# Optimization experiments

Hardware: AMD Instinct MI355X
Metric: run time of the kernel (lower is better)

Reference implementation:

```python
import jax, jax.numpy as jnp
import numpy as np

VOCAB = 50257
EMB = 256
HID = 256
FORGET_BIAS = 1.0


def setup_inputs() -> dict:
    key = jax.random.key(0)
    ks = jax.random.split(key, 8)
    B, T = 16, 256
    s = 0.05
    return {
        "tokens": jax.random.randint(ks[0], (B, T), 0, VOCAB, dtype=jnp.int32),
        # embedding matrix init mimics tf.random_uniform(-1, 1)
        "emb": jax.random.uniform(ks[1], (VOCAB, EMB), jnp.float32, -1.0, 1.0),
        "W1": jax.random.normal(ks[2], (EMB + HID, 4 * HID), jnp.float32) * s,
        "b1": jnp.zeros((4 * HID,), jnp.float32),
        "W2": jax.random.normal(ks[3], (HID + HID, 4 * HID), jnp.float32) * s,
        "b2": jnp.zeros((4 * HID,), jnp.float32),
        "Wout": jax.random.normal(ks[4], (HID, VOCAB), jnp.float32) * s,
        "bout": jnp.zeros((VOCAB,), jnp.float32),
    }


def _lstm_cell(c, h, x, W, b):
    # BasicLSTMCell: gates = [x, h] @ W + b, split i, j, f, o
    g = jnp.concatenate([x, h], axis=-1) @ W + b
    i, j, f, o = jnp.split(g, 4, axis=-1)
    c_new = c * jax.nn.sigmoid(f + FORGET_BIAS) + jax.nn.sigmoid(i) * jnp.tanh(j)
    h_new = jnp.tanh(c_new) * jax.nn.sigmoid(o)
    return c_new, h_new


def reference(tokens, emb, W1, b1, W2, b2, Wout, bout):
    B, T = tokens.shape
    x = emb[tokens]                 # [B, T, EMB] embedding lookup
    x_tm = jnp.swapaxes(x, 0, 1)    # [T, B, EMB] time-major for scan

    def step(carry, xt):
        c1, h1, c2, h2 = carry
        c1, h1 = _lstm_cell(c1, h1, xt, W1, b1)
        c2, h2 = _lstm_cell(c2, h2, h1, W2, b2)
        return (c1, h1, c2, h2), h2

    z = jnp.zeros((B, HID), x.dtype)
    _, hs = jax.lax.scan(step, (z, z, z, z), x_tm)  # hs: [T, B, HID]
    hs = jnp.swapaxes(hs, 0, 1).reshape(-1, HID)    # [B*T, HID] (batch-major flatten as in tf.reshape)
    logits = hs @ Wout + bout                        # [B*T, VOCAB]
    return logits
```

## Files before the change

### kernel.cpp

```cpp
#include <hip/hip_runtime.h>
#include <hip/hip_bf16.h>
#include <stdint.h>

#define BB 16
#define TT 256
#define HH 256
#define EE 256
#define GG 1024
#define VV 50257
#define NN 4096
#define NWK 352
#define NTILE 12608

typedef unsigned short u16;
typedef __attribute__((ext_vector_type(8))) short short8;
typedef __attribute__((ext_vector_type(4))) float f32x4;

__device__ __forceinline__ float sigm(float x){
    float e = __builtin_amdgcn_exp2f(fminf(-x*1.44269504f, 60.0f));
    return 1.0f/(1.0f+e);
}
__device__ __forceinline__ float tanha(float x){
    float e = __builtin_amdgcn_exp2f(fminf(x*2.885390082f, 60.0f));
    return (e-1.0f)/(e+1.0f);
}
__device__ __forceinline__ u16 f2bf(float f){
    uint32_t u = __float_as_uint(f);
    u = (u + 0x7FFFu + ((u>>16)&1u)) >> 16;
    return (u16)u;
}
__device__ __forceinline__ void st32_coh(uint32_t* p, uint32_t v){
    __hip_atomic_store(p, v, __ATOMIC_RELAXED, __HIP_MEMORY_SCOPE_AGENT);
}
__device__ __forceinline__ uint32_t poll_pair(const uint32_t* p){
    uint32_t v = __hip_atomic_load(p, __ATOMIC_RELAXED, __HIP_MEMORY_SCOPE_AGENT);
    while ((v & 0xFFFFu) == 0xFFFFu || (v >> 16) == 0xFFFFu){
        __builtin_amdgcn_s_sleep(1);
        v = __hip_atomic_load(p, __ATOMIC_RELAXED, __HIP_MEMORY_SCOPE_AGENT);
    }
    return v;
}
__device__ __forceinline__ void gl_lds16(const void* g, void* s){
    __builtin_amdgcn_global_load_lds((const __attribute__((address_space(1))) unsigned int*)g,
                                     (__attribute__((address_space(3))) unsigned int*)s, 16, 0, 0);
}

__global__ __launch_bounds__(256) void g1_kernel(const int* __restrict__ tok, const float* __restrict__ emb,
                                                 const float* __restrict__ W1, const float* __restrict__ b1,
                                                 float* __restrict__ G1t){
    __shared__ float xs[64*64];
    __shared__ float wsm[64*64];
    int n0 = blockIdx.x * 64;
    int g0 = blockIdx.y * 64;
    int tid = threadIdx.x;
    int sl = tid & 63;
    int kk = (tid >> 6) * 16;
    int mytok = tok[n0 + sl];
    float acc[4][4] = {};
    int ni = tid & 15, gi = tid >> 4;
    for (int kc = 0; kc < 4; ++kc){
        int k0 = kc*64;
        __syncthreads();
        #pragma unroll
        for (int i4 = 0; i4 < 4; ++i4){
            float4 xv = *(const float4*)(&emb[(size_t)mytok*EE + k0 + kk + i4*4]);
            xs[(kk+i4*4+0)*64 + sl] = xv.x;
            xs[(kk+i4*4+1)*64 + sl] = xv.y;
            xs[(kk+i4*4+2)*64 + sl] = xv.z;
            xs[(kk+i4*4+3)*64 + sl] = xv.w;
        }
        #pragma unroll
        for (int i = 0; i < 16; ++i){
            wsm[(kk+i)*64 + sl] = W1[(size_t)(k0+kk+i)*GG + g0 + sl];
        }
        __syncthreads();
        for (int k = 0; k < 64; ++k){
            float4 av = *(const float4*)(&xs[k*64 + ni*4]);
            float4 bv = *(const float4*)(&wsm[k*64 + gi*4]);
            float a_[4] = {av.x, av.y, av.z, av.w};
            float b_[4] = {bv.x, bv.y, bv.z, bv.w};
            #pragma unroll
            for (int i = 0; i < 4; ++i)
                #pragma unroll
                for (int j = 0; j < 4; ++j)
                    acc[i][j] += a_[i]*b_[j];
        }
    }
    #pragma unroll
    for (int i = 0; i < 4; ++i){
        int n = n0 + ni*4 + i;
        int b = n >> 8;
        int tt_ = n & 255;
        float4 o;
        o.x = acc[i][0] + b1[g0+gi*4+0];
        o.y = acc[i][1] + b1[g0+gi*4+1];
        o.z = acc[i][2] + b1[g0+gi*4+2];
        o.w = acc[i][3] + b1[g0+gi*4+3];
        *(float4*)(&G1t[(size_t)(tt_*16 + b)*GG + g0 + gi*4]) = o;
    }
}

__global__ __launch_bounds__(256) void cast_transpose_wout(const float* __restrict__ Wout,
                                                           u16* __restrict__ WoutT){
    __shared__ u16 tile[64][65];
    int n0 = blockIdx.x * 64;
    int k0 = blockIdx.y * 64;
    int tid = threadIdx.x;
    int r  = tid >> 2;
    int cq = tid & 3;
    #pragma unroll
    for (int i = 0; i < 16; ++i){
        int n = n0 + cq*16 + i;
        float v = (n < VV) ? Wout[(size_t)(k0 + r)*VV + n] : 0.0f;
        tile[cq*16 + i][r] = f2bf(v);
    }
    __syncthreads();
    #pragma unroll
    for (int i4 = 0; i4 < 4; ++i4){
        int kl = cq*16 + i4*4;
        uint2 v;
        v.x = (uint32_t)tile[r][kl+0] | ((uint32_t)tile[r][kl+1] << 16);
        v.y = (uint32_t)tile[r][kl+2] | ((uint32_t)tile[r][kl+3] << 16);
        *(uint2*)(&WoutT[(size_t)(n0 + r)*256 + k0 + kl]) = v;
    }
}

__global__ __launch_bounds__(1024, 8) void fused_kernel(
        const float* __restrict__ G1t, const float* __restrict__ W1,
        const float* __restrict__ W2, const float* __restrict__ b2,
        u16* __restrict__ h1y, u16* __restrict__ h2b,
        const u16* __restrict__ Bt, const float* __restrict__ bout,
        float* __restrict__ out, int* __restrict__ aflag){
    __shared__ __align__(16) char smem[81920];
    const int bid = blockIdx.x;
    const int tid = threadIdx.x;
    uint32_t* h1y32 = (uint32_t*)h1y;
    uint32_t* h2b32 = (uint32_t*)h2b;

    if (bid < 96){
        __builtin_amdgcn_s_setprio(1);
        const int g  = bid & 7;
        const int rr = bid >> 3;
        const int l  = tid & 63;
        const int wv = tid >> 6;

        if (rr < 4){
            const int r1 = rr;
            const int gate = wv >> 2, usub = wv & 3;
            const int colw = gate*HH + 64*r1 + 16*usub;
            short8 wf[8];
            {
                const int col = colw + (l & 15);
                const int kb = (l >> 4) << 3;
                #pragma unroll
                for (int kk = 0; kk < 8; ++kk){
                    short8 s;
                    #pragma unroll
                    for (int j = 0; j < 8; ++j)
                        s[j] = (short)f2bf(W1[(size_t)(HH + kk*32 + kb + j)*GG + col]);
                    wf[kk] = s;
                }
            }
            u16*      hA   = (u16*)smem;
            uint32_t* hA32 = (uint32_t*)smem;
            float*    gm   = (float*)(smem + 1024);
            const int ab = tid >> 5, ap_ = tid & 31;
            float creg0 = 0.f, creg1 = 0.f;

            for (int t = 0; t < TT; ++t){
                float c0 = 0.f, c1 = 0.f;
                if (l < 16){
                    c0 = G1t[((size_t)t*BB + 2*g + 0)*GG + colw + l];
                    c1 = G1t[((size_t)t*BB + 2*g + 1)*GG + colw + l];
                }
                f32x4 acc = {c0, c1, 0.f, 0.f};
                if (t > 0){
                    if (tid < 256){
                        int b = tid >> 7, p = tid & 127;
                        hA32[b*128 + p] = poll_pair(&h1y32[(((size_t)(t-1)*8 + g)*2 + b)*128 + p]);
                    }
                    __syncthreads();
                    const u16* app = hA + (l & 1)*256 + ((l >> 4) << 3);
                    f32x4 acc2 = {0.f, 0.f, 0.f, 0.f};
                    #pragma unroll
                    for (int kk = 0; kk < 4; ++kk){
                        acc  = __builtin_amdgcn_mfma_f32_16x16x32_bf16(*(const short8*)(app + (2*kk  )*32), wf[2*kk  ], acc , 0, 0, 0);
                        acc2 = __builtin_amdgcn_mfma_f32_16x16x32_bf16(*(const short8*)(app + (2*kk+1)*32), wf[2*kk+1], acc2, 0, 0, 0);
                    }
                    acc[0] += acc2[0];
                    acc[1] += acc2[1];
                }
                if (l < 16){
                    gm[(gate*64 + usub*16 + l)*2 + 0] = acc[0];
                    gm[(gate*64 + usub*16 + l)*2 + 1] = acc[1];
                }
                __syncthreads();
                if (tid < 64){
                    int u0 = 2*ap_, u1 = 2*ap_ + 1;
                    float gi0 = gm[(0*64 + u0)*2 + ab], gi1 = gm[(0*64 + u1)*2 + ab];
                    float gj0 = gm[(1*64 + u0)*2 + ab], gj1 = gm[(1*64 + u1)*2 + ab];
                    float gf0 = gm[(2*64 + u0)*2 + ab], gf1 = gm[(2*64 + u1)*2 + ab];
                    float go0 = gm[(3*64 + u0)*2 + ab], go1 = gm[(3*64 + u1)*2 + ab];
                    float cn0 = creg0 * sigm(gf0 + 1.0f) + sigm(gi0)*tanha(gj0);
                    float cn1 = creg1 * sigm(gf1 + 1.0f) + sigm(gi1)*tanha(gj1);
                    float hn0 = tanha(cn0)*sigm(go0);
                    float hn1 = tanha(cn1)*sigm(go1);
                    creg0 = cn0; creg1 = cn1;
                    uint32_t pk = (uint32_t)f2bf(hn0) | ((uint32_t)f2bf(hn1) << 16);
                    st32_coh(&h1y32[(((size_t)t*8 + g)*2 + ab)*128 + 32*r1 + ap_], pk);
                }
                __syncthreads();
            }
        } else {
            const int r2 = rr - 4;
            const int nt = wv >> 1, kh = wv & 1;
            const int gate = nt >> 1, usub = nt & 1;
            const int colw = gate*HH + 32*r2 + 16*usub;
            short8 wf[8];
            {
                const int col = colw + (l & 15);
                const int kb = (l >> 4) << 3;
                #pragma unroll
                for (int kk = 0; kk < 8; ++kk){
                    short8 s;
                    #pragma unroll
                    for (int j = 0; j < 8; ++j)
                        s[j] = (short)f2bf(W2[(size_t)(kh*256 + kk*32 + kb + j)*GG + col]);
                    wf[kk] = s;
                }
            }
            u16*      uB   = (u16*)smem;
            uint32_t* uB32 = (uint32_t*)smem;
            float*    gm   = (float*)(smem + 2048);
            const int ab = tid >> 4, ap_ = tid & 15;
            float creg0 = 0.f, creg1 = 0.f;
            float bvs[4][2];
            if (tid < 32){
                #pragma unroll
                for (int gg = 0; gg < 4; ++gg){
                    bvs[gg][0] = b2[gg*HH + 32*r2 + 2*ap_];
                    bvs[gg][1] = b2[gg*HH + 32*r2 + 2*ap_ + 1];
                }
            }

            for (int tt = 0; tt < TT; ++tt){
                if (tid < 512){
                    int b = tid >> 8, q = tid & 255;
                    uint32_t v;
                    if (q < 128)
                        v = poll_pair(&h1y32[(((size_t)tt*8 + g)*2 + b)*128 + q]);
                    else if (tt > 0)
                        v = poll_pair(&h2b32[((size_t)(2*g + b)*TT + (tt-1))*128 + (q - 128)]);
                    else
                        v = 0;
                    uB32[b*256 + q] = v;
                }
                __syncthreads();
                f32x4 acc = {0.f, 0.f, 0.f, 0.f};
                f32x4 acc2 = {0.f, 0.f, 0.f, 0.f};
                const u16* app = uB + (l & 1)*512 + kh*256 + ((l >> 4) << 3);
                #pragma unroll
                for (int kk = 0; kk < 4; ++kk){
                    acc  = __builtin_amdgcn_mfma_f32_16x16x32_bf16(*(const short8*)(app + (2*kk  )*32), wf[2*kk  ], acc , 0, 0, 0);
                    acc2 = __builtin_amdgcn_mfma_f32_16x16x32_bf16(*(const short8*)(app + (2*kk+1)*32), wf[2*kk+1], acc2, 0, 0, 0);
                }
                acc[0] += acc2[0];
                acc[1] += acc2[1];
                if (l < 16){
                    gm[((gate*32 + usub*16 + l)*2 + 0)*2 + kh] = acc[0];
                    gm[((gate*32 + usub*16 + l)*2 + 1)*2 + kh] = acc[1];
                }
                __syncthreads();
                if (tid < 32){
                    int u0 = 2*ap_, u1 = 2*ap_ + 1;
                    float gi0 = gm[((0*32 + u0)*2 + ab)*2 + 0] + gm[((0*32 + u0)*2 + ab)*2 + 1] + bvs[0][0];
                    float gi1 = gm[((0*32 + u1)*2 + ab)*2 + 0] + gm[((0*32 + u1)*2 + ab)*2 + 1] + bvs[0][1];
                    float gj0 = gm[((1*32 + u0)*2 + ab)*2 + 0] + gm[((1*32 + u0)*2 + ab)*2 + 1] + bvs[1][0];
                    float gj1 = gm[((1*32 + u1)*2 + ab)*2 + 0] + gm[((1*32 + u1)*2 + ab)*2 + 1] + bvs[1][1];
                    float gf0 = gm[((2*32 + u0)*2 + ab)*2 + 0] + gm[((2*32 + u0)*2 + ab)*2 + 1] + bvs[2][0];
                    float gf1 = gm[((2*32 + u1)*2 + ab)*2 + 0] + gm[((2*32 + u1)*2 + ab)*2 + 1] + bvs[2][1];
                    float go0 = gm[((3*32 + u0)*2 + ab)*2 + 0] + gm[((3*32 + u0)*2 + ab)*2 + 1] + bvs[3][0];
                    float go1 = gm[((3*32 + u1)*2 + ab)*2 + 0] + gm[((3*32 + u1)*2 + ab)*2 + 1] + bvs[3][1];
                    float cn0 = creg0 * sigm(gf0 + 1.0f) + sigm(gi0)*tanha(gj0);
                    float cn1 = creg1 * sigm(gf1 + 1.0f) + sigm(gi1)*tanha(gj1);
                    float hn0 = tanha(cn0)*sigm(go0);
                    float hn1 = tanha(cn1)*sigm(go1);
                    creg0 = cn0; creg1 = cn1;
                    uint32_t pk = (uint32_t)f2bf(hn0) | ((uint32_t)f2bf(hn1) << 16);
                    st32_coh(&h2b32[((size_t)(2*g + ab)*TT + tt)*128 + 16*r2 + ap_], pk);
                }
                __syncthreads();
                if (((tt + 1) & 63) == 0 && tid < 32 && (tid & 15) == 0)
                    __hip_atomic_fetch_add(&aflag[(2*g + (tid >> 4))*4 + (tt >> 6)], 1,
                                           __ATOMIC_RELAXED, __HIP_MEMORY_SCOPE_AGENT);
            }
        }
        return;
    }

    const int wid = bid - 96;
    u16* ldsA[2] = {(u16*)smem,           (u16*)(smem + 8192)};
    u16* ldsB[2] = {(u16*)(smem + 16384), (u16*)(smem + 49152)};
    float* ldsF  = (float*)smem;
    const int l = tid & 63, w = tid >> 6;
    const int wm = w >> 2, wn = w & 3;
    const int lr = l & 15, lh = l >> 4;
    const u16* A = h2b;

    #define WSTAGE(c, k0) { \
        if (tid < 512){ \
            int f = tid, row = f >> 3, kp = f & 7, kps = kp ^ (row & 7); \
            gl_lds16(A + (size_t)(m0+row)*256 + (k0) + kps*8, (char*)ldsA[c] + f*16); \
        } \
        _Pragma("unroll") \
        for (int j = 0; j < 2; ++j){ \
            int f = j*1024 + tid, row = f >> 3, kp = f & 7, kps = kp ^ (row & 7); \
            gl_lds16(Bt + (size_t)(n0+row)*256 + (k0) + kps*8, (char*)ldsB[c] + f*16); \
        } }

    for (int s = wid; s < NTILE; s += NWK){
        const int q = s / 3152;
        const int rem = s - q*3152;
        const int nb = rem >> 4, b = rem & 15;
        const int mb = b*4 + q;
        const int m0 = mb*64, n0 = nb*256;

        if (tid == 0){
            while (__hip_atomic_load(&aflag[mb], __ATOMIC_RELAXED, __HIP_MEMORY_SCOPE_AGENT) < 8)
                __builtin_amdgcn_s_sleep(32);
            (void)__hip_atomic_load(&aflag[mb], __ATOMIC_ACQUIRE, __HIP_MEMORY_SCOPE_AGENT);
        }
        __syncthreads();

        f32x4 acc[4];
        #pragma unroll
        for (int nf = 0; nf < 4; ++nf) acc[nf] = (f32x4){0.f,0.f,0.f,0.f};

        WSTAGE(0, 0)
        __syncthreads();
        #pragma unroll
        for (int ks = 0; ks < 4; ++ks){
            const int cur = ks & 1;
            if (ks < 3) WSTAGE(cur^1, (ks+1)*64)
            #pragma unroll
            for (int ksub = 0; ksub < 2; ++ksub){
                const int kp = ksub*4 + lh;
                int arow = wm*16 + lr;
                short8 af = *(const short8*)((const char*)ldsA[cur] + arow*128 + ((kp ^ (arow&7)) << 4));
                #pragma unroll
                for (int nf = 0; nf < 4; ++nf){
                    int brow = wn*64 + nf*16 + lr;
                    short8 bf = *(const short8*)((const char*)ldsB[cur] + brow*128 + ((kp ^ (brow&7)) << 4));
                    acc[nf] = __builtin_amdgcn_mfma_f32_16x16x32_bf16(af, bf, acc[nf], 0, 0, 0);
                }
            }
            __syncthreads();
        }

        #pragma unroll
        for (int nf = 0; nf < 4; ++nf){
            int colL = wn*64 + nf*16 + lr;
            int gcol = n0 + colL;
            float bb = (gcol < VV) ? bout[gcol] : 0.0f;
            #pragma unroll
            for (int r = 0; r < 4; ++r)
                ldsF[(wm*16 + lh*4 + r)*256 + colL] = acc[nf][r] + bb;
        }
        __syncthreads();
        #pragma unroll
        for (int j = 0; j < 4; ++j){
            int f = j*1024 + tid;
            int row = f >> 6;
            int c4 = (f & 63)*4;
            int gcol = n0 + c4;
            f32x4 v = *(const f32x4*)(ldsF + row*256 + c4);
            if (gcol + 3 < VV){
                *(f32x4*)(&out[(size_t)(m0+row)*VV + gcol]) = v;
            } else {
                #pragma unroll
                for (int e = 0; e < 4; ++e)
                    if (gcol + e < VV) out[(size_t)(m0+row)*VV + gcol + e] = v[e];
            }
        }
        __syncthreads();
    }
    #undef WSTAGE
}

extern "C" void kernel_launch(void* const* d_in, const int* in_sizes, int n_in,
                              void* d_out, int out_size, void* d_ws, size_t ws_size,
                              hipStream_t stream) {
    const int*   tok  = (const int*)d_in[0];
    const float* emb  = (const float*)d_in[1];
    const float* W1   = (const float*)d_in[2];
    const float* b1   = (const float*)d_in[3];
    const float* W2   = (const float*)d_in[4];
    const float* b2   = (const float*)d_in[5];
    const float* Wout = (const float*)d_in[6];
    const float* bout = (const float*)d_in[7];
    float* out = (float*)d_out;
    char* ws = (char*)d_ws;

    int*   aflag = (int*)  (ws);
    u16*   h1y   = (u16*)  (ws + 4096);
    u16*   h2b   = (u16*)  (ws + 4096 + 2097152);
    float* G1t   = (float*)(ws + 4096 + 4194304);
    u16*   WoutT = (u16*)  (ws + 4096 + 20971520);

    hipMemsetAsync(ws, 0, 4096, stream);
    hipMemsetAsync(ws + 4096, 0xFF, 4194304, stream);
    g1_kernel<<<dim3(64, 16), 256, 0, stream>>>(tok, emb, W1, b1, G1t);
    cast_transpose_wout<<<dim3(792, 4), 256, 0, stream>>>(Wout, WoutT);
    fused_kernel<<<96 + NWK, 1024, 0, stream>>>(G1t, W1, W2, b2, h1y, h2b,
                                                WoutT, bout, out, aflag);
}
```

Baseline: 943.6 us.

## Fuse Wout cast-transpose into fused kernel with column-stationary GEMM blocks

Removes the separate cast_transpose_wout launch. Each of 197 worker blocks now owns one 256-column slice of Wout, converts and transposes it into WoutT itself while the LSTM recurrence runs, then loops over all 64 row blocks grouped by time quarter. A quarter is processed only after all 16 batch flags for it are set. This keeps the B slice hot in cache and hides the transpose behind the recurrence, but it makes quarter synchronization coarser and reduces the number of workers, which may cut parallelism in the output GEMM. The LDS epilogue stride is also padded to 258.

New measurement: 1.160 ms. 1.23x slower.

```diff
diff --git a/kernel.cpp b/kernel.cpp
--- a/kernel.cpp
+++ b/kernel.cpp
@@ -9,8 +9,7 @@
 #define GG 1024
 #define VV 50257
 #define NN 4096
-#define NWK 352
-#define NTILE 12608
+#define NWK 197
 
 typedef unsigned short u16;
 typedef __attribute__((ext_vector_type(8))) short short8;
@@ -100,37 +99,13 @@
     }
 }
 
-__global__ __launch_bounds__(256) void cast_transpose_wout(const float* __restrict__ Wout,
-                                                           u16* __restrict__ WoutT){
-    __shared__ u16 tile[64][65];
-    int n0 = blockIdx.x * 64;
-    int k0 = blockIdx.y * 64;
-    int tid = threadIdx.x;
-    int r  = tid >> 2;
-    int cq = tid & 3;
-    #pragma unroll
-    for (int i = 0; i < 16; ++i){
-        int n = n0 + cq*16 + i;
-        float v = (n < VV) ? Wout[(size_t)(k0 + r)*VV + n] : 0.0f;
-        tile[cq*16 + i][r] = f2bf(v);
-    }
-    __syncthreads();
-    #pragma unroll
-    for (int i4 = 0; i4 < 4; ++i4){
-        int kl = cq*16 + i4*4;
-        uint2 v;
-        v.x = (uint32_t)tile[r][kl+0] | ((uint32_t)tile[r][kl+1] << 16);
-        v.y = (uint32_t)tile[r][kl+2] | ((uint32_t)tile[r][kl+3] << 16);
-        *(uint2*)(&WoutT[(size_t)(n0 + r)*256 + k0 + kl]) = v;
-    }
-}
-
 __global__ __launch_bounds__(1024, 8) void fused_kernel(
         const float* __restrict__ G1t, const float* __restrict__ W1,
         const float* __restrict__ W2, const float* __restrict__ b2,
+        const float* __restrict__ Wout, u16* __restrict__ WoutT,
         u16* __restrict__ h1y, u16* __restrict__ h2b,
-        const u16* __restrict__ Bt, const float* __restrict__ bout,
-        float* __restrict__ out, int* __restrict__ aflag){
+        const float* __restrict__ bout, float* __restrict__ out,
+        int* __restrict__ aflag){
     __shared__ __align__(16) char smem[81920];
     const int bid = blockIdx.x;
     const int tid = threadIdx.x;
@@ -299,6 +274,32 @@
     }
 
     const int wid = bid - 96;
+    const int n0 = wid*256;
+
+    {
+        u16* tile = (u16*)smem;
+        for (int kc = 0; kc < 4; ++kc){
+            int k0 = kc*64;
+            #pragma unroll
+            for (int i = 0; i < 16; ++i){
+                int idx = i*1024 + tid;
+                int kl = idx >> 8, nl = idx & 255;
+                int n = n0 + nl;
+                float v = (n < VV) ? Wout[(size_t)(k0+kl)*VV + n] : 0.0f;
+                tile[nl*66 + kl] = f2bf(v);
+            }
+            __syncthreads();
+            #pragma unroll
+            for (int i = 0; i < 8; ++i){
+                int idx = i*1024 + tid;
+                int nl = idx >> 5, kw = idx & 31;
+                uint32_t pk = (uint32_t)tile[nl*66 + kw*2] | ((uint32_t)tile[nl*66 + kw*2 + 1] << 16);
+                *(uint32_t*)&WoutT[(size_t)(n0+nl)*256 + k0 + kw*2] = pk;
+            }
+            __syncthreads();
+        }
+    }
+
     u16* ldsA[2] = {(u16*)smem,           (u16*)(smem + 8192)};
     u16* ldsB[2] = {(u16*)(smem + 16384), (u16*)(smem + 49152)};
     float* ldsF  = (float*)smem;
@@ -306,6 +307,7 @@
     const int wm = w >> 2, wn = w & 3;
     const int lr = l & 15, lh = l >> 4;
     const u16* A = h2b;
+    const u16* Bt = WoutT;
 
     #define WSTAGE(c, k0) { \
         if (tid < 512){ \
@@ -318,71 +320,72 @@
             gl_lds16(Bt + (size_t)(n0+row)*256 + (k0) + kps*8, (char*)ldsB[c] + f*16); \
         } }
 
-    for (int s = wid; s < NTILE; s += NWK){
-        const int q = s / 3152;
-        const int rem = s - q*3152;
-        const int nb = rem >> 4, b = rem & 15;
-        const int mb = b*4 + q;
-        const int m0 = mb*64, n0 = nb*256;
-
+    for (int q = 0; q < 4; ++q){
         if (tid == 0){
-            while (__hip_atomic_load(&aflag[mb], __ATOMIC_RELAXED, __HIP_MEMORY_SCOPE_AGENT) < 8)
-                __builtin_amdgcn_s_sleep(32);
-            (void)__hip_atomic_load(&aflag[mb], __ATOMIC_ACQUIRE, __HIP_MEMORY_SCOPE_AGENT);
+            #pragma unroll
+            for (int b = 0; b < 16; ++b)
+                while (__hip_atomic_load(&aflag[b*4 + q], __ATOMIC_RELAXED, __HIP_MEMORY_SCOPE_AGENT) < 8)
+                    __builtin_amdgcn_s_sleep(32);
+            (void)__hip_atomic_load(&aflag[q], __ATOMIC_ACQUIRE, __HIP_MEMORY_SCOPE_AGENT);
         }
         __syncthreads();
 
-        f32x4 acc[4];
-        #pragma unroll
-        for (int nf = 0; nf < 4; ++nf) acc[nf] = (f32x4){0.f,0.f,0.f,0.f};
-
-        WSTAGE(0, 0)
-        __syncthreads();
-        #pragma unroll
-        for (int ks = 0; ks < 4; ++ks){
-            const int cur = ks & 1;
-            if (ks < 3) WSTAGE(cur^1, (ks+1)*64)
-            #pragma unroll
-            for (int ksub = 0; ksub < 2; ++ksub){
-                const int kp = ksub*4 + lh;
-                int arow = wm*16 + lr;
-                short8 af = *(const short8*)((const char*)ldsA[cur] + arow*128 + ((kp ^ (arow&7)) << 4));
-                #pragma unroll
-                for (int nf = 0; nf < 4; ++nf){
-                    int brow = wn*64 + nf*16 + lr;
-                    short8 bf = *(const short8*)((const char*)ldsB[cur] + brow*128 + ((kp ^ (brow&7)) << 4));
-                    acc[nf] = __builtin_amdgcn_mfma_f32_16x16x32_bf16(af, bf, acc[nf], 0, 0, 0);
-                }
-            }
+        for (int b = 0; b < 16; ++b){
+            const int mb = b*4 + q;
+            const int m0 = mb*64;
+
+            f32x4 acc[4];
+            #pragma unroll
+            for (int nf = 0; nf < 4; ++nf) acc[nf] = (f32x4){0.f,0.f,0.f,0.f};
+
+            WSTAGE(0, 0)
             __syncthreads();
-        }
-
-        #pragma unroll
-        for (int nf = 0; nf < 4; ++nf){
-            int colL = wn*64 + nf*16 + lr;
-            int gcol = n0 + colL;
-            float bb = (gcol < VV) ? bout[gcol] : 0.0f;
-            #pragma unroll
-            for (int r = 0; r < 4; ++r)
-                ldsF[(wm*16 + lh*4 + r)*256 + colL] = acc[nf][r] + bb;
-        }
-        __syncthreads();
-        #pragma unroll
-        for (int j = 0; j < 4; ++j){
-            int f = j*1024 + tid;
-            int row = f >> 6;
-            int c4 = (f & 63)*4;
-            int gcol = n0 + c4;
-            f32x4 v = *(const f32x4*)(ldsF + row*256 + c4);
-            if (gcol + 3 < VV){
-                *(f32x4*)(&out[(size_t)(m0+row)*VV + gcol]) = v;
-            } else {
-                #pragma unroll
-                for (int e = 0; e < 4; ++e)
-                    if (gcol + e < VV) out[(size_t)(m0+row)*VV + gcol + e] = v[e];
-            }
-        }
-        __syncthreads();
+            #pragma unroll
+            for (int ks = 0; ks < 4; ++ks){
+                const int cur = ks & 1;
+                if (ks < 3) WSTAGE(cur^1, (ks+1)*64)
+                #pragma unroll
+                for (int ksub = 0; ksub < 2; ++ksub){
+                    const int kp = ksub*4 + lh;
+                    int arow = wm*16 + lr;
+                    short8 af = *(const short8*)((const char*)ldsA[cur] + arow*128 + ((kp ^ (arow&7)) << 4));
+                    #pragma unroll
+                    for (int nf = 0; nf < 4; ++nf){
+                        int brow = wn*64 + nf*16 + lr;
+                        short8 bf = *(const short8*)((const char*)ldsB[cur] + brow*128 + ((kp ^ (brow&7)) << 4));
+                        acc[nf] = __builtin_amdgcn_mfma_f32_16x16x32_bf16(af, bf, acc[nf], 0, 0, 0);
+                    }
+                }
+                __syncthreads();
+            }
+
+            #pragma unroll
+            for (int nf = 0; nf < 4; ++nf){
+                int colL = wn*64 + nf*16 + lr;
+                int gcol = n0 + colL;
+                float bb = (gcol < VV) ? bout[gcol] : 0.0f;
+                #pragma unroll
+                for (int r = 0; r < 4; ++r)
+                    ldsF[(wm*16 + lh*4 + r)*258 + colL] = acc[nf][r] + bb;
+            }
+            __syncthreads();
+            #pragma unroll
+            for (int j = 0; j < 4; ++j){
+                int f = j*1024 + tid;
+                int row = f >> 6;
+                int c4 = (f & 63)*4;
+                int gcol = n0 + c4;
+                f32x4 v = *(const f32x4*)(ldsF + row*258 + c4);
+                if (gcol + 3 < VV){
+                    *(f32x4*)(&out[(size_t)(m0+row)*VV + gcol]) = v;
+                } else {
+                    #pragma unroll
+                    for (int e = 0; e < 4; ++e)
+                        if (gcol + e < VV) out[(size_t)(m0+row)*VV + gcol + e] = v[e];
+                }
+            }
+            __syncthreads();
+        }
     }
     #undef WSTAGE
 }
@@ -410,7 +413,6 @@
     hipMemsetAsync(ws, 0, 4096, stream);
     hipMemsetAsync(ws + 4096, 0xFF, 4194304, stream);
     g1_kernel<<<dim3(64, 16), 256, 0, stream>>>(tok, emb, W1, b1, G1t);
-    cast_transpose_wout<<<dim3(792, 4), 256, 0, stream>>>(Wout, WoutT);
-    fused_kernel<<<96 + NWK, 1024, 0, stream>>>(G1t, W1, W2, b2, h1y, h2b,
-                                                WoutT, bout, out, aflag);
-}
+    fused_kernel<<<96 + NWK, 1024, 0, stream>>>(G1t, W1, W2, b2, Wout, WoutT,
+                                                h1y, h2b, bout, out, aflag);
+}
```
